# Kernel tuning notes

Hardware: AMD Instinct MI355X
Metric: run time of the kernel (lower is better)

Reference implementation:

```python
import jax, jax.numpy as jnp
import numpy as np

N_NODES = 100000
N_EDGES = 1600000
D_IN = 256
D_OUT = 128


def setup_inputs() -> dict:
    key = jax.random.key(0)
    k1, k2, k3, k4, k5, k6 = jax.random.split(key, 6)
    in_feature = jax.random.normal(k1, (N_NODES, D_IN), dtype=jnp.float32)
    edge_rows = jax.random.randint(k2, (N_EDGES,), 0, N_NODES, dtype=jnp.int32)
    edge_cols = jax.random.randint(k3, (N_EDGES,), 0, N_NODES, dtype=jnp.int32)
    edge_vals = jax.random.uniform(k4, (N_EDGES,), dtype=jnp.float32)
    weight = jax.random.normal(k5, (D_IN, D_OUT), dtype=jnp.float32) * (1.0 / np.sqrt(D_IN))
    bias = jax.random.normal(k6, (D_OUT,), dtype=jnp.float32) * 0.01
    return {"in_feature": in_feature, "edge_rows": edge_rows, "edge_cols": edge_cols,
            "edge_vals": edge_vals, "weight": weight, "bias": bias}


def reference(in_feature, edge_rows, edge_cols, edge_vals, weight, bias):
    # Dense feature transform: [N, D_in] @ [D_in, D_out]
    support = in_feature @ weight
    # Sparse adjacency SpMM in COO form:
    # out[r] = sum over edges (r, c, v) of v * support[c]
    msgs = edge_vals[:, None] * support[edge_cols]  # [E, D_out]
    output = jax.ops.segment_sum(msgs, edge_rows, num_segments=in_feature.shape[0])
    return output + bias
```

## Files before the change

kernel.cpp:

```cpp
#include <hip/hip_runtime.h>
#include <hip/hip_bf16.h>

#define N_NODES 100000
#define N_EDGES 1600000
#define D_IN 256
#define D_OUT 128
#define NB16 6250
#define CHUNK 8192
#define NCHUNK ((N_EDGES + CHUNK - 1) / CHUNK)
#define PCAP16 512

typedef __attribute__((ext_vector_type(8))) short bf16x8;
typedef __attribute__((ext_vector_type(4))) float f32x4;

__device__ inline ushort f2bf(float f) {
    __hip_bfloat16 h = __float2bfloat16(f);
    union { __hip_bfloat16 h; ushort u; } cvt;
    cvt.h = h;
    return cvt.u;
}

__device__ inline float bfe(ushort u) { return __uint_as_float((uint)u << 16); }

__global__ __launch_bounds__(256) void gemm_kernel(const float* __restrict__ X,
                                                   const float* __restrict__ W,
                                                   ushort* __restrict__ supp) {
    __shared__ ushort Wt[128 * 256];

    const int tid = threadIdx.x;
    for (int idx = tid; idx < 128 * 128; idx += 256) {
        int n  = idx & 127;
        int k  = (idx >> 7) * 2;
        float w0 = W[(size_t)k * D_OUT + n];
        float w1 = W[(size_t)(k + 1) * D_OUT + n];
        uint b = ((uint)f2bf(w1) << 16) | f2bf(w0);
        int slot = ((k >> 3) ^ (n & 7));
        uint off = (uint)n * 256 + (uint)slot * 8 + (k & 7);
        *(uint*)&Wt[off] = b;
    }
    __syncthreads();

    const int w = tid >> 6;
    const int l = tid & 63;
    const int c = l & 15;
    const int g = l >> 4;
    const int rbase = blockIdx.x * 128 + w * 32;

    int r0 = rbase + c;       if (r0 > N_NODES - 1) r0 = N_NODES - 1;
    int r1 = rbase + 16 + c;  if (r1 > N_NODES - 1) r1 = N_NODES - 1;
    const float* x0 = X + (size_t)r0 * D_IN + g * 8;
    const float* x1 = X + (size_t)r1 * D_IN + g * 8;

    f32x4 acc[2][8];
    #pragma unroll
    for (int mi = 0; mi < 2; ++mi)
        #pragma unroll
        for (int j = 0; j < 8; ++j)
            acc[mi][j] = (f32x4){0.f, 0.f, 0.f, 0.f};

    #pragma unroll
    for (int s = 0; s < 8; ++s) {
        float4 a0l = *(const float4*)(x0 + s * 32);
        float4 a0h = *(const float4*)(x0 + s * 32 + 4);
        float4 a1l = *(const float4*)(x1 + s * 32);
        float4 a1h = *(const float4*)(x1 + s * 32 + 4);
        bf16x8 a0, a1;
        a0[0] = (short)f2bf(a0l.x); a0[1] = (short)f2bf(a0l.y);
        a0[2] = (short)f2bf(a0l.z); a0[3] = (short)f2bf(a0l.w);
        a0[4] = (short)f2bf(a0h.x); a0[5] = (short)f2bf(a0h.y);
        a0[6] = (short)f2bf(a0h.z); a0[7] = (short)f2bf(a0h.w);
        a1[0] = (short)f2bf(a1l.x); a1[1] = (short)f2bf(a1l.y);
        a1[2] = (short)f2bf(a1l.z); a1[3] = (short)f2bf(a1l.w);
        a1[4] = (short)f2bf(a1h.x); a1[5] = (short)f2bf(a1h.y);
        a1[6] = (short)f2bf(a1h.z); a1[7] = (short)f2bf(a1h.w);

        #pragma unroll
        for (int j = 0; j < 8; ++j) {
            const bf16x8 b = *(const bf16x8*)
                &Wt[(uint)(16 * j + c) * 256 + (uint)(((4 * s + g) ^ (c & 7)) * 8)];
            acc[0][j] = __builtin_amdgcn_mfma_f32_16x16x32_bf16(a0, b, acc[0][j], 0, 0, 0);
            acc[1][j] = __builtin_amdgcn_mfma_f32_16x16x32_bf16(a1, b, acc[1][j], 0, 0, 0);
        }
    }

    #pragma unroll
    for (int mi = 0; mi < 2; ++mi) {
        int rb = rbase + mi * 16 + g * 4;
        #pragma unroll
        for (int reg = 0; reg < 4; ++reg) {
            int r = rb + reg;
            if (r < N_NODES) {
                #pragma unroll
                for (int j = 0; j < 8; ++j)
                    supp[(size_t)r * D_OUT + 16 * j + c] = f2bf(acc[mi][j][reg]);
            }
        }
    }
}

__global__ __launch_bounds__(256) void part_kernel(const int4* __restrict__ rows4,
                                                   const int4* __restrict__ cols4,
                                                   const float4* __restrict__ vals4,
                                                   int* __restrict__ gcursor,
                                                   float2* __restrict__ edata) {
    __shared__ int cnt[NB16];
    const int tid = threadIdx.x;
    for (int i = tid; i < NB16; i += 256) cnt[i] = 0;
    __syncthreads();

    const int i4base = blockIdx.x * (CHUNK / 4);
    #pragma unroll
    for (int j = 0; j < 8; ++j) {
        int i4 = i4base + j * 256 + tid;
        if (i4 < N_EDGES / 4) {
            int4 r = rows4[i4];
            atomicAdd(&cnt[r.x >> 4], 1);
            atomicAdd(&cnt[r.y >> 4], 1);
            atomicAdd(&cnt[r.z >> 4], 1);
            atomicAdd(&cnt[r.w >> 4], 1);
        }
    }
    __syncthreads();
    for (int i = tid; i < NB16; i += 256) {
        int c = cnt[i];
        cnt[i] = c ? atomicAdd(&gcursor[i], c) : 0;
    }
    __syncthreads();
    #pragma unroll
    for (int j = 0; j < 8; ++j) {
        int i4 = i4base + j * 256 + tid;
        if (i4 < N_EDGES / 4) {
            int4 r = rows4[i4];
            int4 cc = cols4[i4];
            float4 v = vals4[i4];
            int b, slot;
            b = r.x >> 4; slot = atomicAdd(&cnt[b], 1);
            if (slot < PCAP16)
                edata[(size_t)b * PCAP16 + slot] = make_float2(__int_as_float(((r.x & 15) << 17) | cc.x), v.x);
            b = r.y >> 4; slot = atomicAdd(&cnt[b], 1);
            if (slot < PCAP16)
                edata[(size_t)b * PCAP16 + slot] = make_float2(__int_as_float(((r.y & 15) << 17) | cc.y), v.y);
            b = r.z >> 4; slot = atomicAdd(&cnt[b], 1);
            if (slot < PCAP16)
                edata[(size_t)b * PCAP16 + slot] = make_float2(__int_as_float(((r.z & 15) << 17) | cc.z), v.z);
            b = r.w >> 4; slot = atomicAdd(&cnt[b], 1);
            if (slot < PCAP16)
                edata[(size_t)b * PCAP16 + slot] = make_float2(__int_as_float(((r.w & 15) << 17) | cc.w), v.w);
        }
    }
}

__global__ __launch_bounds__(256) void spmm16_kernel(const int* __restrict__ bcount,
                                                     const float2* __restrict__ edata,
                                                     const ushort* __restrict__ supp,
                                                     const float* __restrict__ bias,
                                                     float* __restrict__ out) {
    __shared__ float acc[4 * 16 * 128];
    const int tid = threadIdx.x;

    for (int i = tid; i < 2048; i += 256)
        *(float4*)&acc[i * 4] = *(const float4*)&bias[(i & 31) * 4];
    __syncthreads();

    const int w = tid >> 6;
    const int lane = tid & 63;
    const int bkt = blockIdx.x * 4 + w;

    if (bkt < NB16) {
        int n = bcount[bkt];
        if (n > PCAP16) n = PCAP16;
        const float2* ed = edata + (size_t)bkt * PCAP16;
        float* accw = &acc[w * 2048];

        int i = 0;
        for (; i + 4 <= n; i += 4) {
            float2 e0 = ed[i];
            float2 e1 = ed[i + 1];
            float2 e2 = ed[i + 2];
            float2 e3 = ed[i + 3];
            uint p0 = (uint)__float_as_int(e0.x);
            uint p1 = (uint)__float_as_int(e1.x);
            uint p2 = (uint)__float_as_int(e2.x);
            uint p3 = (uint)__float_as_int(e3.x);
            const ushort* s0 = supp + (size_t)(p0 & 0x1FFFF) * D_OUT;
            const ushort* s1 = supp + (size_t)(p1 & 0x1FFFF) * D_OUT;
            const ushort* s2 = supp + (size_t)(p2 & 0x1FFFF) * D_OUT;
            const ushort* s3 = supp + (size_t)(p3 & 0x1FFFF) * D_OUT;
            float lo0 = bfe(s0[lane]), hi0 = bfe(s0[lane + 64]);
            float lo1 = bfe(s1[lane]), hi1 = bfe(s1[lane + 64]);
            float lo2 = bfe(s2[lane]), hi2 = bfe(s2[lane + 64]);
            float lo3 = bfe(s3[lane]), hi3 = bfe(s3[lane + 64]);
            int r0 = (int)(p0 >> 17) * 128 + lane;
            int r1 = (int)(p1 >> 17) * 128 + lane;
            int r2 = (int)(p2 >> 17) * 128 + lane;
            int r3 = (int)(p3 >> 17) * 128 + lane;
            accw[r0]      += e0.y * lo0;
            accw[r0 + 64] += e0.y * hi0;
            accw[r1]      += e1.y * lo1;
            accw[r1 + 64] += e1.y * hi1;
            accw[r2]      += e2.y * lo2;
            accw[r2 + 64] += e2.y * hi2;
            accw[r3]      += e3.y * lo3;
            accw[r3 + 64] += e3.y * hi3;
        }
        for (; i < n; ++i) {
            float2 e0 = ed[i];
            uint p0 = (uint)__float_as_int(e0.x);
            const ushort* s0 = supp + (size_t)(p0 & 0x1FFFF) * D_OUT;
            float lo0 = bfe(s0[lane]), hi0 = bfe(s0[lane + 64]);
            int r0 = (int)(p0 >> 17) * 128 + lane;
            accw[r0]      += e0.y * lo0;
            accw[r0 + 64] += e0.y * hi0;
        }
    }
    __syncthreads();

    const int row0 = blockIdx.x * 64;
    for (int i = tid; i < 2048; i += 256) {
        int r = row0 + (i >> 5);
        if (r < N_NODES)
            *(float4*)&out[(size_t)r * D_OUT + (i & 31) * 4] = *(const float4*)&acc[i * 4];
    }
}

extern "C" void kernel_launch(void* const* d_in, const int* in_sizes, int n_in,
                              void* d_out, int out_size, void* d_ws, size_t ws_size,
                              hipStream_t stream) {
    const float* X    = (const float*)d_in[0];
    const int*   rows = (const int*)  d_in[1];
    const int*   cols = (const int*)  d_in[2];
    const float* vals = (const float*)d_in[3];
    const float* W    = (const float*)d_in[4];
    const float* bias = (const float*)d_in[5];
    float* out = (float*)d_out;

    char* p = (char*)d_ws;
    auto take = [&](size_t bytes) {
        char* r = p;
        p += (bytes + 255) & ~(size_t)255;
        return r;
    };
    ushort* supp    = (ushort*)take((size_t)N_NODES * D_OUT * 2);
    float2* edata   = (float2*)take((size_t)NB16 * PCAP16 * 8);
    int*    gcursor = (int*)   take((size_t)NB16 * 4);

    gemm_kernel<<<(N_NODES + 127) / 128, 256, 0, stream>>>(X, W, supp);

    hipMemsetAsync(gcursor, 0, (size_t)NB16 * 4, stream);
    part_kernel<<<NCHUNK, 256, 0, stream>>>((const int4*)rows, (const int4*)cols,
                                            (const float4*)vals, gcursor, edata);

    spmm16_kernel<<<(NB16 + 3) / 4, 256, 0, stream>>>(gcursor, edata, supp, bias, out);
}
```

Measured before the change: 367.9 us.

## Sort bucketed edges by row and use register-accumulating row-per-wave SpMM

Adds a per-bucket counting sort that groups edges by destination row into a CSR-like layout with per-row offsets and counts. The SpMM then assigns one wave per row, accumulates in registers with FMAs, and gathers packed bf16 pairs with a single 32-bit load per lane. This removes shared-memory read-modify-write accumulation and the bias/LDS staging, at the cost of an extra kernel pass over the edge data and more workspace.

```diff
diff --git a/kernel.cpp b/kernel.cpp
--- a/kernel.cpp
+++ b/kernel.cpp
@@ -20,7 +20,8 @@
     return cvt.u;
 }
 
-__device__ inline float bfe(ushort u) { return __uint_as_float((uint)u << 16); }
+__device__ inline float bflo(uint u) { return __uint_as_float(u << 16); }
+__device__ inline float bfhi(uint u) { return __uint_as_float(u & 0xffff0000u); }
 
 __global__ __launch_bounds__(256) void gemm_kernel(const float* __restrict__ X,
                                                    const float* __restrict__ W,
@@ -150,77 +151,89 @@
     }
 }
 
-__global__ __launch_bounds__(256) void spmm16_kernel(const int* __restrict__ bcount,
+__global__ __launch_bounds__(256) void sort16_kernel(const int* __restrict__ bcount,
                                                      const float2* __restrict__ edata,
-                                                     const ushort* __restrict__ supp,
-                                                     const float* __restrict__ bias,
-                                                     float* __restrict__ out) {
-    __shared__ float acc[4 * 16 * 128];
+                                                     float2* __restrict__ edata2,
+                                                     int2* __restrict__ row_info) {
+    __shared__ int bins[4][16];
+    __shared__ int cur[4][16];
     const int tid = threadIdx.x;
-
-    for (int i = tid; i < 2048; i += 256)
-        *(float4*)&acc[i * 4] = *(const float4*)&bias[(i & 31) * 4];
-    __syncthreads();
-
     const int w = tid >> 6;
     const int lane = tid & 63;
     const int bkt = blockIdx.x * 4 + w;
-
-    if (bkt < NB16) {
-        int n = bcount[bkt];
-        if (n > PCAP16) n = PCAP16;
-        const float2* ed = edata + (size_t)bkt * PCAP16;
-        float* accw = &acc[w * 2048];
-
-        int i = 0;
-        for (; i + 4 <= n; i += 4) {
-            float2 e0 = ed[i];
-            float2 e1 = ed[i + 1];
-            float2 e2 = ed[i + 2];
-            float2 e3 = ed[i + 3];
-            uint p0 = (uint)__float_as_int(e0.x);
-            uint p1 = (uint)__float_as_int(e1.x);
-            uint p2 = (uint)__float_as_int(e2.x);
-            uint p3 = (uint)__float_as_int(e3.x);
-            const ushort* s0 = supp + (size_t)(p0 & 0x1FFFF) * D_OUT;
-            const ushort* s1 = supp + (size_t)(p1 & 0x1FFFF) * D_OUT;
-            const ushort* s2 = supp + (size_t)(p2 & 0x1FFFF) * D_OUT;
-            const ushort* s3 = supp + (size_t)(p3 & 0x1FFFF) * D_OUT;
-            float lo0 = bfe(s0[lane]), hi0 = bfe(s0[lane + 64]);
-            float lo1 = bfe(s1[lane]), hi1 = bfe(s1[lane + 64]);
-            float lo2 = bfe(s2[lane]), hi2 = bfe(s2[lane + 64]);
-            float lo3 = bfe(s3[lane]), hi3 = bfe(s3[lane + 64]);
-            int r0 = (int)(p0 >> 17) * 128 + lane;
-            int r1 = (int)(p1 >> 17) * 128 + lane;
-            int r2 = (int)(p2 >> 17) * 128 + lane;
-            int r3 = (int)(p3 >> 17) * 128 + lane;
-            accw[r0]      += e0.y * lo0;
-            accw[r0 + 64] += e0.y * hi0;
-            accw[r1]      += e1.y * lo1;
-            accw[r1 + 64] += e1.y * hi1;
-            accw[r2]      += e2.y * lo2;
-            accw[r2 + 64] += e2.y * hi2;
-            accw[r3]      += e3.y * lo3;
-            accw[r3 + 64] += e3.y * hi3;
-        }
-        for (; i < n; ++i) {
-            float2 e0 = ed[i];
-            uint p0 = (uint)__float_as_int(e0.x);
-            const ushort* s0 = supp + (size_t)(p0 & 0x1FFFF) * D_OUT;
-            float lo0 = bfe(s0[lane]), hi0 = bfe(s0[lane + 64]);
-            int r0 = (int)(p0 >> 17) * 128 + lane;
-            accw[r0]      += e0.y * lo0;
-            accw[r0 + 64] += e0.y * hi0;
-        }
-    }
-    __syncthreads();
-
-    const int row0 = blockIdx.x * 64;
-    for (int i = tid; i < 2048; i += 256) {
-        int r = row0 + (i >> 5);
-        if (r < N_NODES)
-            *(float4*)&out[(size_t)r * D_OUT + (i & 31) * 4] = *(const float4*)&acc[i * 4];
-    }
+    if (bkt >= NB16) return;
+
+    int n = bcount[bkt];
+    if (n > PCAP16) n = PCAP16;
+    const int base = bkt * PCAP16;
+    const float2* ed = edata + base;
+
+    if (lane < 16) bins[w][lane] = 0;
+    for (int i = lane; i < n; i += 64) {
+        uint pk = (uint)__float_as_int(ed[i].x);
+        atomicAdd(&bins[w][pk >> 17], 1);
+    }
+    if (lane < 16) {
+        int c = bins[w][lane];
+        int x = c;
+        #pragma unroll
+        for (int off = 1; off < 16; off <<= 1) {
+            int t = __shfl_up(x, off, 64);
+            if (lane >= off) x += t;
+        }
+        int excl = x - c;
+        cur[w][lane] = excl;
+        row_info[bkt * 16 + lane] = make_int2(base + excl, c);
+    }
+    for (int i = lane; i < n; i += 64) {
+        float2 rec = ed[i];
+        uint pk = (uint)__float_as_int(rec.x);
+        int slot = atomicAdd(&cur[w][pk >> 17], 1);
+        edata2[base + slot] = make_float2(__int_as_float((int)(pk & 0x1FFFF)), rec.y);
+    }
+}
+
+__global__ __launch_bounds__(256) void spmm_kernel(const int2* __restrict__ row_info,
+                                                   const float2* __restrict__ edata,
+                                                   const ushort* __restrict__ supp,
+                                                   const float* __restrict__ bias,
+                                                   float* __restrict__ out) {
+    const int wave = threadIdx.x >> 6;
+    const int lane = threadIdx.x & 63;
+    const int row = blockIdx.x * 4 + wave;
+    if (row >= N_NODES) return;
+    const int d0 = lane * 2;
+
+    float2 acc = *(const float2*)&bias[d0];
+    int2 se = row_info[row];
+    int e = se.x;
+    const int end = se.x + se.y;
+
+    for (; e + 4 <= end; e += 4) {
+        float2 e0 = edata[e];
+        float2 e1 = edata[e + 1];
+        float2 e2 = edata[e + 2];
+        float2 e3 = edata[e + 3];
+        uint s0 = *(const uint*)(supp + (size_t)__float_as_int(e0.x) * D_OUT + d0);
+        uint s1 = *(const uint*)(supp + (size_t)__float_as_int(e1.x) * D_OUT + d0);
+        uint s2 = *(const uint*)(supp + (size_t)__float_as_int(e2.x) * D_OUT + d0);
+        uint s3 = *(const uint*)(supp + (size_t)__float_as_int(e3.x) * D_OUT + d0);
+        acc.x = fmaf(e0.y, bflo(s0), acc.x);
+        acc.y = fmaf(e0.y, bfhi(s0), acc.y);
+        acc.x = fmaf(e1.y, bflo(s1), acc.x);
+        acc.y = fmaf(e1.y, bfhi(s1), acc.y);
+        acc.x = fmaf(e2.y, bflo(s2), acc.x);
+        acc.y = fmaf(e2.y, bfhi(s2), acc.y);
+        acc.x = fmaf(e3.y, bflo(s3), acc.x);
+        acc.y = fmaf(e3.y, bfhi(s3), acc.y);
+    }
+    for (; e < end; ++e) {
+        float2 ed = edata[e];
+        uint s = *(const uint*)(supp + (size_t)__float_as_int(ed.x) * D_OUT + d0);
+        acc.x = fmaf(ed.y, bflo(s), acc.x);
+        acc.y = fmaf(ed.y, bfhi(s), acc.y);
+    }
+    *(float2*)&out[(size_t)row * D_OUT + d0] = acc;
 }
 
 extern "C" void kernel_launch(void* const* d_in, const int* in_sizes, int n_in,
@@ -240,9 +253,11 @@
         p += (bytes + 255) & ~(size_t)255;
         return r;
     };
-    ushort* supp    = (ushort*)take((size_t)N_NODES * D_OUT * 2);
-    float2* edata   = (float2*)take((size_t)NB16 * PCAP16 * 8);
-    int*    gcursor = (int*)   take((size_t)NB16 * 4);
+    ushort* supp     = (ushort*)take((size_t)N_NODES * D_OUT * 2);
+    float2* edata    = (float2*)take((size_t)NB16 * PCAP16 * 8);
+    float2* edata2   = (float2*)take((size_t)NB16 * PCAP16 * 8);
+    int2*   row_info = (int2*)  take((size_t)N_NODES * 8);
+    int*    gcursor  = (int*)   take((size_t)NB16 * 4);
 
     gemm_kernel<<<(N_NODES + 127) / 128, 256, 0, stream>>>(X, W, supp);
 
@@ -250,5 +265,7 @@
     part_kernel<<<NCHUNK, 256, 0, stream>>>((const int4*)rows, (const int4*)cols,
                                             (const float4*)vals, gcursor, edata);
 
-    spmm16_kernel<<<(NB16 + 3) / 4, 256, 0, stream>>>(gcursor, edata, supp, bias, out);
-}
+    sort16_kernel<<<(NB16 + 3) / 4, 256, 0, stream>>>(gcursor, edata, edata2, row_info);
+
+    spmm_kernel<<<(N_NODES + 3) / 4, 256, 0, stream>>>(row_info, edata2, supp, bias, out);
+}
```

Result: faster. 335.4 us (-8.8%).
